# Optimization experiments

Hardware: AMD Instinct MI355X
Metric: run time of the kernel (lower is better)

Reference implementation:

```python
import jax, jax.numpy as jnp
import numpy as np

D_MODEL = 1024
H = 16
D_K = D_MODEL // H
B, S = 4, 2048


def setup_inputs() -> dict:
    key = jax.random.key(0)
    ks = jax.random.split(key, 12)
    std = 1.0 / np.sqrt(D_MODEL)
    inp = {
        "q": jax.random.normal(ks[0], (B, S, D_MODEL), dtype=jnp.float32),
        "k": jax.random.normal(ks[1], (B, S, D_MODEL), dtype=jnp.float32),
        "v": jax.random.normal(ks[2], (B, S, D_MODEL), dtype=jnp.float32),
        "mask": jnp.tril(jnp.ones((S, S), dtype=jnp.int32))[None, None],  # [1,1,S,S] causal
        "w_q": jax.random.normal(ks[3], (D_MODEL, D_MODEL), dtype=jnp.float32) * std,
        "b_q": jax.random.normal(ks[4], (D_MODEL,), dtype=jnp.float32) * std,
        "w_k": jax.random.normal(ks[5], (D_MODEL, D_MODEL), dtype=jnp.float32) * std,
        "b_k": jax.random.normal(ks[6], (D_MODEL,), dtype=jnp.float32) * std,
        "w_v": jax.random.normal(ks[7], (D_MODEL, D_MODEL), dtype=jnp.float32) * std,
        "b_v": jax.random.normal(ks[8], (D_MODEL,), dtype=jnp.float32) * std,
        "w_o": jax.random.normal(ks[9], (D_MODEL, D_MODEL), dtype=jnp.float32) * std,
        "b_o": jax.random.normal(ks[10], (D_MODEL,), dtype=jnp.float32) * std,
    }
    return inp


def reference(q, k, v, mask, w_q, b_q, w_k, b_k, w_v, b_v, w_o, b_o):
    b, s, _ = q.shape
    # linear projections (torch Linear: x @ W^T + b)
    query = q @ w_q.T + b_q
    key_ = k @ w_k.T + b_k
    value = v @ w_v.T + b_v
    # [B,S,D] -> [B,H,S,Dk]
    query = query.reshape(b, s, H, D_K).transpose(0, 2, 1, 3)
    key_ = key_.reshape(b, -1, H, D_K).transpose(0, 2, 1, 3)
    value = value.reshape(b, -1, H, D_K).transpose(0, 2, 1, 3)
    scores = jnp.einsum("bhqd,bhkd->bhqk", query, key_) / jnp.sqrt(jnp.float32(D_K))
    scores = jnp.where(mask == 0, jnp.float32(-1e9), scores)
    attn = jax.nn.softmax(scores, axis=-1)
    out = jnp.einsum("bhqk,bhkd->bhqd", attn, value)
    out = out.transpose(0, 2, 1, 3).reshape(b, s, D_MODEL)
    return out @ w_o.T + b_o
```

## Files before the change

### kernel.cpp

```cpp
#include <hip/hip_runtime.h>


typedef _Float16 h8 __attribute__((ext_vector_type(8)));
typedef float f32x4 __attribute__((ext_vector_type(4)));
typedef float f32x16 __attribute__((ext_vector_type(16)));

#define S_LEN 2048
#define DM 1024
#define DK 64

struct H2 { _Float16 h, l; };
__device__ __forceinline__ H2 split2(float v) {
  H2 r; r.h = (_Float16)v; r.l = (_Float16)(v - (float)r.h); return r;
}
__device__ __forceinline__ unsigned int pack2(float a, float b) {
  union { _Float16 h[2]; unsigned int u; } x;
  x.h[0] = (_Float16)a; x.h[1] = (_Float16)b;
  return x.u;
}

#define GLOAD16(gp, lp)                                                        \
  __builtin_amdgcn_global_load_lds(                                            \
      (const __attribute__((address_space(1))) void*)(gp),                     \
      (__attribute__((address_space(3))) void*)(lp), 16, 0, 0)

__global__ __launch_bounds__(256)
void presplit(const float* __restrict__ X, _Float16* __restrict__ Hi,
              _Float16* __restrict__ Lo, int n8) {
  const int i = blockIdx.x * 256 + threadIdx.x;
  if (i >= n8) return;
  const float4 a = ((const float4*)X)[2 * i];
  const float4 b = ((const float4*)X)[2 * i + 1];
  h8 hv, lv;
  H2 s;
  s = split2(a.x); hv[0] = s.h; lv[0] = s.l;
  s = split2(a.y); hv[1] = s.h; lv[1] = s.l;
  s = split2(a.z); hv[2] = s.h; lv[2] = s.l;
  s = split2(a.w); hv[3] = s.h; lv[3] = s.l;
  s = split2(b.x); hv[4] = s.h; lv[4] = s.l;
  s = split2(b.y); hv[5] = s.h; lv[5] = s.l;
  s = split2(b.z); hv[6] = s.h; lv[6] = s.l;
  s = split2(b.w); hv[7] = s.h; lv[7] = s.l;
  *(h8*)&Hi[(size_t)i * 8] = hv;
  *(h8*)&Lo[(size_t)i * 8] = lv;
}

template<int OUT_MODE>
__global__ __launch_bounds__(256)
void gemm_ps(const _Float16* __restrict__ Xhi, const _Float16* __restrict__ Xlo,
             const _Float16* __restrict__ Whi, const _Float16* __restrict__ Wlo,
             const float* __restrict__ bias,
             _Float16* __restrict__ Yhi, _Float16* __restrict__ Ylo,
             float* __restrict__ Yf) {
  __shared__ _Float16 lds[2][4][128 * 32];
  const int tid = threadIdx.x;
  const int m0 = blockIdx.x * 128, n0 = blockIdx.y * 128;
  const int wid = tid >> 6, lane = tid & 63;
  const int wm = (wid >> 1) * 64, wn = (wid & 1) * 64;
  const int l15 = lane & 15, lg = lane >> 4;
  const _Float16* gsrc = (wid == 0) ? Xhi : (wid == 1) ? Xlo : (wid == 2) ? Whi : Wlo;
  const int rbase = (wid < 2) ? m0 : n0;
  const int rowoff = lane >> 2, coloff = (lane & 3) * 8;
  f32x4 acc[4][4] = {};

  auto stage = [&](int buf, int kt) {
    const int k0 = kt * 32;
#pragma unroll
    for (int c = 0; c < 8; ++c) {
      GLOAD16(&gsrc[(size_t)(rbase + c * 16 + rowoff) * DM + k0 + coloff],
              &lds[buf][wid][c * 512]);
    }
  };

  stage(0, 0);
  __syncthreads();
  for (int kt = 0; kt < 32; ++kt) {
    const int buf = kt & 1;
    if (kt + 1 < 32) stage(buf ^ 1, kt + 1);
    h8 a_h[4], a_l[4], b_h[4], b_l[4];
#pragma unroll
    for (int i = 0; i < 4; ++i) {
      const int ra = (wm + i * 16 + l15) * 32 + lg * 8;
      const int rb = (wn + i * 16 + l15) * 32 + lg * 8;
      a_h[i] = *(const h8*)&lds[buf][0][ra];
      a_l[i] = *(const h8*)&lds[buf][1][ra];
      b_h[i] = *(const h8*)&lds[buf][2][rb];
      b_l[i] = *(const h8*)&lds[buf][3][rb];
    }
    __builtin_amdgcn_s_setprio(1);
#pragma unroll
    for (int mi = 0; mi < 4; ++mi)
#pragma unroll
      for (int ni = 0; ni < 4; ++ni) {
        acc[mi][ni] = __builtin_amdgcn_mfma_f32_16x16x32_f16(a_h[mi], b_h[ni], acc[mi][ni], 0, 0, 0);
        acc[mi][ni] = __builtin_amdgcn_mfma_f32_16x16x32_f16(a_h[mi], b_l[ni], acc[mi][ni], 0, 0, 0);
        acc[mi][ni] = __builtin_amdgcn_mfma_f32_16x16x32_f16(a_l[mi], b_h[ni], acc[mi][ni], 0, 0, 0);
      }
    __builtin_amdgcn_s_setprio(0);
    __syncthreads();
  }
#pragma unroll
  for (int mi = 0; mi < 4; ++mi)
#pragma unroll
    for (int ni = 0; ni < 4; ++ni)
#pragma unroll
      for (int j = 0; j < 4; ++j) {
        const int rg = m0 + wm + mi * 16 + lg * 4 + j;
        const int cg = n0 + wn + ni * 16 + l15;
        const float v = acc[mi][ni][j] + bias[cg];
        if constexpr (OUT_MODE == 0) {
          H2 s = split2(v);
          Yhi[(size_t)rg * DM + cg] = s.h;
          Ylo[(size_t)rg * DM + cg] = s.l;
        } else {
          Yf[(size_t)rg * DM + cg] = v;
        }
      }
}

__global__ __launch_bounds__(256)
void mha_vtrans(const float* __restrict__ Vp,
                _Float16* __restrict__ Vthi, _Float16* __restrict__ Vtlo) {
  __shared__ float tile[64 * 65];
  const int bh = blockIdx.y, s0 = blockIdx.x * 64;
  const int b = bh >> 4, h = bh & 15;
  const int t = threadIdx.x;
  const int row = t >> 2, cg = (t & 3) * 16;
  const size_t inbase = ((size_t)(b * S_LEN + s0 + row)) * DM + h * DK + cg;
#pragma unroll
  for (int i = 0; i < 4; ++i) {
    const float4 v = *(const float4*)&Vp[inbase + i * 4];
    tile[row * 65 + cg + i * 4 + 0] = v.x;
    tile[row * 65 + cg + i * 4 + 1] = v.y;
    tile[row * 65 + cg + i * 4 + 2] = v.z;
    tile[row * 65 + cg + i * 4 + 3] = v.w;
  }
  __syncthreads();
  const int drow = t >> 2, sg = (t & 3) * 16;
  h8 hv0, hv1, lv0, lv1;
#pragma unroll
  for (int i = 0; i < 8; ++i) {
    H2 a = split2(tile[(sg + i) * 65 + drow]);
    hv0[i] = a.h; lv0[i] = a.l;
    H2 c = split2(tile[(sg + 8 + i) * 65 + drow]);
    hv1[i] = c.h; lv1[i] = c.l;
  }
  const size_t ob = ((size_t)bh * DK + drow) * S_LEN + s0 + sg;
  *(h8*)&Vthi[ob] = hv0;
  *(h8*)&Vthi[ob + 8] = hv1;
  *(h8*)&Vtlo[ob] = lv0;
  *(h8*)&Vtlo[ob + 8] = lv1;
}

__global__ __launch_bounds__(64)
void mha_attn(const _Float16* __restrict__ Qhi, const _Float16* __restrict__ Qlo,
              const _Float16* __restrict__ Khi, const _Float16* __restrict__ Klo,
              const _Float16* __restrict__ Vthi, const _Float16* __restrict__ Vtlo,
              _Float16* __restrict__ Ohi, _Float16* __restrict__ Olo) {
  const int lane = threadIdx.x;
  const int l31 = lane & 31, hi = lane >> 5;
  const int hwid = blockIdx.x + (blockIdx.y << 5);
  const int logical = (hwid & 7) * 256 + (hwid >> 3);
  const int r = logical & 31;
  const int bh = logical >> 5;
  const int fq = 63 - r;
  const int b = bh >> 4, h = bh & 15;
  const size_t rowbase = (size_t)b * S_LEN * DM + h * DK;
  const size_t vbase = (size_t)bh * DK * S_LEN;

  h8 qh_r[4], ql_r[4], qh_f[4], ql_f[4];
#pragma unroll
  for (int ks = 0; ks < 4; ++ks) {
    const size_t offr = rowbase + (size_t)(r * 32 + l31) * DM + ks * 16 + hi * 8;
    const size_t offf = rowbase + (size_t)(fq * 32 + l31) * DM + ks * 16 + hi * 8;
    qh_r[ks] = *(const h8*)&Qhi[offr]; ql_r[ks] = *(const h8*)&Qlo[offr];
    qh_f[ks] = *(const h8*)&Qhi[offf]; ql_f[ks] = *(const h8*)&Qlo[offf];
  }
  f32x16 po0r = {}, po1r = {}, po0f = {}, po1f = {};
  float m_r = -1e30f, l_r = 0.0f, m_f = -1e30f, l_f = 0.0f;

  auto loadK = [&](int t, h8 (&kh)[4], h8 (&kl)[4]) {
    const int c0 = t * 32;
#pragma unroll
    for (int ks = 0; ks < 4; ++ks) {
      const size_t koff = rowbase + (size_t)(c0 + l31) * DM + ks * 16 + hi * 8;
      kh[ks] = *(const h8*)&Khi[koff];
      kl[ks] = *(const h8*)&Klo[koff];
    }
  };

  auto smax_pv = [&](const f32x16& sA, const f32x16& sB, bool diag,
                     float& m, float& l, f32x16& po0, f32x16& po1,
                     const h8 (&vh)[2][2], const h8 (&vl)[2][2]) {
    float p[16];
    float tmax = -3e38f;
#pragma unroll
    for (int rr = 0; rr < 16; ++rr) {
      const int kvr = (rr & 3) + 8 * (rr >> 2) + 4 * hi;
      float sv = (sA[rr] + sB[rr]) * 0.125f;
      if (diag && kvr > l31) sv = -1e30f;
      p[rr] = sv;
      tmax = fmaxf(tmax, sv);
    }
    tmax = fmaxf(tmax, __shfl_xor(tmax, 32, 64));
    if (!__all(tmax <= m + 8.0f)) {
      const float mnew = fmaxf(m, tmax);
      const float alpha = __expf(m - mnew);
      l *= alpha;
      po0 = po0 * alpha;
      po1 = po1 * alpha;
      m = mnew;
    }
    float tsum = 0.0f;
#pragma unroll
    for (int rr = 0; rr < 16; ++rr) { p[rr] = __expf(p[rr] - m); tsum += p[rr]; }
    tsum += __shfl_xor(tsum, 32, 64);
    l += tsum;
    unsigned int pw[8], qw[8];
#pragma unroll
    for (int g = 0; g < 8; ++g) pw[g] = pack2(p[2 * g], p[2 * g + 1]);
#pragma unroll
    for (int g = 0; g < 8; ++g) qw[g] = (unsigned int)__shfl_xor((int)pw[g], 32, 64);
    __builtin_amdgcn_s_setprio(1);
#pragma unroll
    for (int cks = 0; cks < 2; ++cks) {
      union { unsigned int u[4]; h8 v; } bp;
      if (hi == 0) {
        bp.u[0] = pw[4 * cks];     bp.u[1] = pw[4 * cks + 1];
        bp.u[2] = qw[4 * cks];     bp.u[3] = qw[4 * cks + 1];
      } else {
        bp.u[0] = qw[4 * cks + 2]; bp.u[1] = qw[4 * cks + 3];
        bp.u[2] = pw[4 * cks + 2]; bp.u[3] = pw[4 * cks + 3];
      }
      po0 = __builtin_amdgcn_mfma_f32_32x32x16_f16(vh[cks][0], bp.v, po0, 0, 0, 0);
      po0 = __builtin_amdgcn_mfma_f32_32x32x16_f16(vl[cks][0], bp.v, po0, 0, 0, 0);
      po1 = __builtin_amdgcn_mfma_f32_32x32x16_f16(vh[cks][1], bp.v, po1, 0, 0, 0);
      po1 = __builtin_amdgcn_mfma_f32_32x32x16_f16(vl[cks][1], bp.v, po1, 0, 0, 0);
    }
    __builtin_amdgcn_s_setprio(0);
  };

  auto body = [&](int t, const h8 (&kh)[4], const h8 (&kl)[4],
                  h8 (&nkh)[4], h8 (&nkl)[4]) {
    const int c0 = t * 32;
    h8 vh[2][2], vl[2][2];
#pragma unroll
    for (int cks = 0; cks < 2; ++cks) {
      const size_t voff = vbase + (size_t)l31 * S_LEN + c0 + cks * 16 + hi * 8;
      vh[cks][0] = *(const h8*)&Vthi[voff];
      vl[cks][0] = *(const h8*)&Vtlo[voff];
      vh[cks][1] = *(const h8*)&Vthi[voff + (size_t)32 * S_LEN];
      vl[cks][1] = *(const h8*)&Vtlo[voff + (size_t)32 * S_LEN];
    }
    if (t + 1 <= fq) loadK(t + 1, nkh, nkl);
    {
      f32x16 sA = {}, sB = {};
      __builtin_amdgcn_s_setprio(1);
#pragma unroll
      for (int ks = 0; ks < 4; ++ks) {
        sA = __builtin_amdgcn_mfma_f32_32x32x16_f16(kh[ks], qh_f[ks], sA, 0, 0, 0);
        sB = __builtin_amdgcn_mfma_f32_32x32x16_f16(kh[ks], ql_f[ks], sB, 0, 0, 0);
        sB = __builtin_amdgcn_mfma_f32_32x32x16_f16(kl[ks], qh_f[ks], sB, 0, 0, 0);
      }
      __builtin_amdgcn_s_setprio(0);
      smax_pv(sA, sB, t == fq, m_f, l_f, po0f, po1f, vh, vl);
    }
    if (t <= r) {
      f32x16 sA = {}, sB = {};
      __builtin_amdgcn_s_setprio(1);
#pragma unroll
      for (int ks = 0; ks < 4; ++ks) {
        sA = __builtin_amdgcn_mfma_f32_32x32x16_f16(kh[ks], qh_r[ks], sA, 0, 0, 0);
        sB = __builtin_amdgcn_mfma_f32_32x32x16_f16(kh[ks], ql_r[ks], sB, 0, 0, 0);
        sB = __builtin_amdgcn_mfma_f32_32x32x16_f16(kl[ks], qh_r[ks], sB, 0, 0, 0);
      }
      __builtin_amdgcn_s_setprio(0);
      smax_pv(sA, sB, t == r, m_r, l_r, po0r, po1r, vh, vl);
    }
  };

  h8 khA[4], klA[4], khB[4], klB[4];
  loadK(0, khA, klA);
  int t = 0;
  while (true) {
    body(t, khA, klA, khB, klB);
    ++t; if (t > fq) break;
    body(t, khB, klB, khA, klA);
    ++t; if (t > fq) break;
  }

  __shared__ float lds_o[32 * 65];
  auto writeO = [&](int qt, float l, const f32x16& po0, const f32x16& po1) {
    const float invl = 1.0f / l;
#pragma unroll
    for (int rr = 0; rr < 16; ++rr) {
      const int dl = (rr & 3) + 8 * (rr >> 2) + 4 * hi;
      lds_o[l31 * 65 + dl] = po0[rr] * invl;
      lds_o[l31 * 65 + 32 + dl] = po1[rr] * invl;
    }
    __syncthreads();
    const size_t ob = ((size_t)b * S_LEN + qt * 32) * DM + h * DK;
    for (int r2 = 0; r2 < 32; ++r2) {
      H2 s = split2(lds_o[r2 * 65 + lane]);
      Ohi[ob + (size_t)r2 * DM + lane] = s.h;
      Olo[ob + (size_t)r2 * DM + lane] = s.l;
    }
    __syncthreads();
  };
  writeO(fq, l_f, po0f, po1f);
  writeO(r, l_r, po0r, po1r);
}

extern "C" void kernel_launch(void* const* d_in, const int* in_sizes, int n_in,
                              void* d_out, int out_size, void* d_ws, size_t ws_size,
                              hipStream_t stream) {
  const float* q   = (const float*)d_in[0];
  const float* k   = (const float*)d_in[1];
  const float* v   = (const float*)d_in[2];
  const float* w_q = (const float*)d_in[4];
  const float* b_q = (const float*)d_in[5];
  const float* w_k = (const float*)d_in[6];
  const float* b_k = (const float*)d_in[7];
  const float* w_v = (const float*)d_in[8];
  const float* b_v = (const float*)d_in[9];
  const float* w_o = (const float*)d_in[10];
  const float* b_o = (const float*)d_in[11];

  const size_t NIN = (size_t)8192 * 1024;
  const size_t NW  = (size_t)1024 * 1024;
  const size_t SZH = NIN * sizeof(_Float16);
  char* ws = (char*)d_ws;
  _Float16* b1 = (_Float16*)(ws + 0 * SZH);
  _Float16* b2 = (_Float16*)(ws + 2 * SZH);
  _Float16* b3 = (_Float16*)(ws + 4 * SZH);
  char*     b4 = ws + 6 * SZH;

  _Float16* Xhi = b1;            _Float16* Xlo = b1 + NIN;
  _Float16* Qph = b2;            _Float16* Qpl = b2 + NIN;
  _Float16* Kph = b3;            _Float16* Kpl = b3 + NIN;
  float*    Vp  = (float*)b4;
  _Float16* Vth = (_Float16*)b1; _Float16* Vtl = (_Float16*)b1 + NIN;
  _Float16* Oh  = (_Float16*)b4; _Float16* Ol  = (_Float16*)b4 + NIN;
  _Float16* Wdh = (_Float16*)d_out; _Float16* Wdl = (_Float16*)d_out + NW;
  _Float16* Woh = (_Float16*)b2;    _Float16* Wol = (_Float16*)b2 + NW;

  const int NIN8 = (int)(NIN / 8), NW8 = (int)(NW / 8);
  dim3 gg(64, 8);

  presplit<<<4096, 256, 0, stream>>>(q, Xhi, Xlo, NIN8);
  presplit<<<512, 256, 0, stream>>>(w_q, Wdh, Wdl, NW8);
  gemm_ps<0><<<gg, 256, 0, stream>>>(Xhi, Xlo, Wdh, Wdl, b_q, Qph, Qpl, nullptr);
  presplit<<<4096, 256, 0, stream>>>(k, Xhi, Xlo, NIN8);
  presplit<<<512, 256, 0, stream>>>(w_k, Wdh, Wdl, NW8);
  gemm_ps<0><<<gg, 256, 0, stream>>>(Xhi, Xlo, Wdh, Wdl, b_k, Kph, Kpl, nullptr);
  presplit<<<4096, 256, 0, stream>>>(v, Xhi, Xlo, NIN8);
  presplit<<<512, 256, 0, stream>>>(w_v, Wdh, Wdl, NW8);
  gemm_ps<1><<<gg, 256, 0, stream>>>(Xhi, Xlo, Wdh, Wdl, b_v, nullptr, nullptr, Vp);
  mha_vtrans<<<dim3(32, 64), 256, 0, stream>>>(Vp, Vth, Vtl);
  mha_attn<<<dim3(32, 64), 64, 0, stream>>>(Qph, Qpl, Kph, Kpl, Vth, Vtl, Oh, Ol);
  presplit<<<512, 256, 0, stream>>>(w_o, Woh, Wol, NW8);
  gemm_ps<1><<<gg, 256, 0, stream>>>(Oh, Ol, Woh, Wol, b_o, nullptr, nullptr, (float*)d_out);
}
```

Measured before the change: 636.4 us.

## Share K/V tiles across four waves via double-buffered swizzled LDS in attention

```diff
diff --git a/kernel.cpp b/kernel.cpp
--- a/kernel.cpp
+++ b/kernel.cpp
@@ -152,22 +152,54 @@
   *(h8*)&Vtlo[ob + 8] = lv1;
 }
 
-__global__ __launch_bounds__(64)
+__global__ __launch_bounds__(256)
 void mha_attn(const _Float16* __restrict__ Qhi, const _Float16* __restrict__ Qlo,
               const _Float16* __restrict__ Khi, const _Float16* __restrict__ Klo,
               const _Float16* __restrict__ Vthi, const _Float16* __restrict__ Vtlo,
               _Float16* __restrict__ Ohi, _Float16* __restrict__ Olo) {
-  const int lane = threadIdx.x;
+  __shared__ int4 smem4[2080];
+  char* smem = (char*)smem4;
+  const int tid = threadIdx.x;
+  const int w = tid >> 6, lane = tid & 63;
   const int l31 = lane & 31, hi = lane >> 5;
-  const int hwid = blockIdx.x + (blockIdx.y << 5);
-  const int logical = (hwid & 7) * 256 + (hwid >> 3);
-  const int r = logical & 31;
-  const int bh = logical >> 5;
+  const int hwid = blockIdx.x + (blockIdx.y << 3);
+  const int logical = (hwid & 7) * 64 + (hwid >> 3);
+  const int bh = logical >> 3, pg = logical & 7;
+  const int r = pg * 4 + w;
   const int fq = 63 - r;
+  const int TMAX = 63 - pg * 4;
   const int b = bh >> 4, h = bh & 15;
   const size_t rowbase = (size_t)b * S_LEN * DM + h * DK;
   const size_t vbase = (size_t)bh * DK * S_LEN;
 
+  const int krow = tid >> 3, kq = tid & 7;
+  const int vd = tid >> 2, vj = tid & 3;
+
+  auto kaddr = [&](int buf, int row, int slot) {
+    return buf * 8192 + row * 256 + ((slot ^ (row & 15)) << 4);
+  };
+  auto vaddr = [&](int buf, int d, int slot) {
+    return 16384 + buf * 8192 + d * 128 + ((slot ^ (d & 7)) << 4);
+  };
+
+  h8 sKh, sKl, sVh, sVl;
+  auto stage_load = [&](int t) {
+    const int c0 = t * 32;
+    const size_t ko = rowbase + (size_t)(c0 + krow) * DM + kq * 8;
+    const size_t vo = vbase + (size_t)vd * S_LEN + c0 + vj * 8;
+    sKh = *(const h8*)&Khi[ko];
+    sKl = *(const h8*)&Klo[ko];
+    sVh = *(const h8*)&Vthi[vo];
+    sVl = *(const h8*)&Vtlo[vo];
+  };
+  auto stage_write = [&](int buf) {
+    *(h8*)(smem + kaddr(buf, krow, kq)) = sKh;
+    *(h8*)(smem + kaddr(buf, krow, kq + 8)) = sKl;
+    *(h8*)(smem + vaddr(buf, vd, vj)) = sVh;
+    *(h8*)(smem + vaddr(buf, vd, vj + 4)) = sVl;
+  };
+
+  stage_load(0);
   h8 qh_r[4], ql_r[4], qh_f[4], ql_f[4];
 #pragma unroll
   for (int ks = 0; ks < 4; ++ks) {
@@ -176,22 +208,14 @@
     qh_r[ks] = *(const h8*)&Qhi[offr]; ql_r[ks] = *(const h8*)&Qlo[offr];
     qh_f[ks] = *(const h8*)&Qhi[offf]; ql_f[ks] = *(const h8*)&Qlo[offf];
   }
+  stage_write(0);
+  __syncthreads();
+
   f32x16 po0r = {}, po1r = {}, po0f = {}, po1f = {};
   float m_r = -1e30f, l_r = 0.0f, m_f = -1e30f, l_f = 0.0f;
 
-  auto loadK = [&](int t, h8 (&kh)[4], h8 (&kl)[4]) {
-    const int c0 = t * 32;
-#pragma unroll
-    for (int ks = 0; ks < 4; ++ks) {
-      const size_t koff = rowbase + (size_t)(c0 + l31) * DM + ks * 16 + hi * 8;
-      kh[ks] = *(const h8*)&Khi[koff];
-      kl[ks] = *(const h8*)&Klo[koff];
-    }
-  };
-
-  auto smax_pv = [&](const f32x16& sA, const f32x16& sB, bool diag,
-                     float& m, float& l, f32x16& po0, f32x16& po1,
-                     const h8 (&vh)[2][2], const h8 (&vl)[2][2]) {
+  auto smax_pv = [&](int buf, const f32x16& sA, const f32x16& sB, bool diag,
+                     float& m, float& l, f32x16& po0, f32x16& po1) {
     float p[16];
     float tmax = -3e38f;
 #pragma unroll
@@ -232,80 +256,79 @@
         bp.u[0] = qw[4 * cks + 2]; bp.u[1] = qw[4 * cks + 3];
         bp.u[2] = pw[4 * cks + 2]; bp.u[3] = pw[4 * cks + 3];
       }
-      po0 = __builtin_amdgcn_mfma_f32_32x32x16_f16(vh[cks][0], bp.v, po0, 0, 0, 0);
-      po0 = __builtin_amdgcn_mfma_f32_32x32x16_f16(vl[cks][0], bp.v, po0, 0, 0, 0);
-      po1 = __builtin_amdgcn_mfma_f32_32x32x16_f16(vh[cks][1], bp.v, po1, 0, 0, 0);
-      po1 = __builtin_amdgcn_mfma_f32_32x32x16_f16(vl[cks][1], bp.v, po1, 0, 0, 0);
+      const h8 vh0 = *(const h8*)(smem + vaddr(buf, l31, 2 * cks + hi));
+      const h8 vl0 = *(const h8*)(smem + vaddr(buf, l31, 4 + 2 * cks + hi));
+      const h8 vh1 = *(const h8*)(smem + vaddr(buf, l31 + 32, 2 * cks + hi));
+      const h8 vl1 = *(const h8*)(smem + vaddr(buf, l31 + 32, 4 + 2 * cks + hi));
+      po0 = __builtin_amdgcn_mfma_f32_32x32x16_f16(vh0, bp.v, po0, 0, 0, 0);
+      po0 = __builtin_amdgcn_mfma_f32_32x32x16_f16(vl0, bp.v, po0, 0, 0, 0);
+      po1 = __builtin_amdgcn_mfma_f32_32x32x16_f16(vh1, bp.v, po1, 0, 0, 0);
+      po1 = __builtin_amdgcn_mfma_f32_32x32x16_f16(vl1, bp.v, po1, 0, 0, 0);
     }
     __builtin_amdgcn_s_setprio(0);
   };
 
-  auto body = [&](int t, const h8 (&kh)[4], const h8 (&kl)[4],
-                  h8 (&nkh)[4], h8 (&nkl)[4]) {
-    const int c0 = t * 32;
-    h8 vh[2][2], vl[2][2];
-#pragma unroll
-    for (int cks = 0; cks < 2; ++cks) {
-      const size_t voff = vbase + (size_t)l31 * S_LEN + c0 + cks * 16 + hi * 8;
-      vh[cks][0] = *(const h8*)&Vthi[voff];
-      vl[cks][0] = *(const h8*)&Vtlo[voff];
-      vh[cks][1] = *(const h8*)&Vthi[voff + (size_t)32 * S_LEN];
-      vl[cks][1] = *(const h8*)&Vtlo[voff + (size_t)32 * S_LEN];
-    }
-    if (t + 1 <= fq) loadK(t + 1, nkh, nkl);
-    {
-      f32x16 sA = {}, sB = {};
-      __builtin_amdgcn_s_setprio(1);
+  for (int t = 0; t <= TMAX; ++t) {
+    const int buf = t & 1;
+    if (t < TMAX) stage_load(t + 1);
+    if (t <= fq) {
+      h8 kh[4], kl[4];
 #pragma unroll
       for (int ks = 0; ks < 4; ++ks) {
-        sA = __builtin_amdgcn_mfma_f32_32x32x16_f16(kh[ks], qh_f[ks], sA, 0, 0, 0);
-        sB = __builtin_amdgcn_mfma_f32_32x32x16_f16(kh[ks], ql_f[ks], sB, 0, 0, 0);
-        sB = __builtin_amdgcn_mfma_f32_32x32x16_f16(kl[ks], qh_f[ks], sB, 0, 0, 0);
-      }
-      __builtin_amdgcn_s_setprio(0);
-      smax_pv(sA, sB, t == fq, m_f, l_f, po0f, po1f, vh, vl);
-    }
-    if (t <= r) {
-      f32x16 sA = {}, sB = {};
-      __builtin_amdgcn_s_setprio(1);
-#pragma unroll
-      for (int ks = 0; ks < 4; ++ks) {
-        sA = __builtin_amdgcn_mfma_f32_32x32x16_f16(kh[ks], qh_r[ks], sA, 0, 0, 0);
-        sB = __builtin_amdgcn_mfma_f32_32x32x16_f16(kh[ks], ql_r[ks], sB, 0, 0, 0);
-        sB = __builtin_amdgcn_mfma_f32_32x32x16_f16(kl[ks], qh_r[ks], sB, 0, 0, 0);
-      }
-      __builtin_amdgcn_s_setprio(0);
-      smax_pv(sA, sB, t == r, m_r, l_r, po0r, po1r, vh, vl);
-    }
-  };
-
-  h8 khA[4], klA[4], khB[4], klB[4];
-  loadK(0, khA, klA);
-  int t = 0;
-  while (true) {
-    body(t, khA, klA, khB, klB);
-    ++t; if (t > fq) break;
-    body(t, khB, klB, khA, klA);
-    ++t; if (t > fq) break;
-  }
-
-  __shared__ float lds_o[32 * 65];
+        kh[ks] = *(const h8*)(smem + kaddr(buf, l31, 2 * ks + hi));
+        kl[ks] = *(const h8*)(smem + kaddr(buf, l31, 8 + 2 * ks + hi));
+      }
+      {
+        f32x16 sA = {}, sB = {};
+        __builtin_amdgcn_s_setprio(1);
+#pragma unroll
+        for (int ks = 0; ks < 4; ++ks) {
+          sA = __builtin_amdgcn_mfma_f32_32x32x16_f16(kh[ks], qh_f[ks], sA, 0, 0, 0);
+          sB = __builtin_amdgcn_mfma_f32_32x32x16_f16(kh[ks], ql_f[ks], sB, 0, 0, 0);
+          sB = __builtin_amdgcn_mfma_f32_32x32x16_f16(kl[ks], qh_f[ks], sB, 0, 0, 0);
+        }
+        __builtin_amdgcn_s_setprio(0);
+        smax_pv(buf, sA, sB, t == fq, m_f, l_f, po0f, po1f);
+      }
+      if (t <= r) {
+        f32x16 sA = {}, sB = {};
+        __builtin_amdgcn_s_setprio(1);
+#pragma unroll
+        for (int ks = 0; ks < 4; ++ks) {
+          sA = __builtin_amdgcn_mfma_f32_32x32x16_f16(kh[ks], qh_r[ks], sA, 0, 0, 0);
+          sB = __builtin_amdgcn_mfma_f32_32x32x16_f16(kh[ks], ql_r[ks], sB, 0, 0, 0);
+          sB = __builtin_amdgcn_mfma_f32_32x32x16_f16(kl[ks], qh_r[ks], sB, 0, 0, 0);
+        }
+        __builtin_amdgcn_s_setprio(0);
+        smax_pv(buf, sA, sB, t == r, m_r, l_r, po0r, po1r);
+      }
+    }
+    __syncthreads();
+    if (t < TMAX) stage_write(buf ^ 1);
+    __syncthreads();
+  }
+
+  unsigned int* outl = (unsigned int*)(smem + w * 8320);
   auto writeO = [&](int qt, float l, const f32x16& po0, const f32x16& po1) {
     const float invl = 1.0f / l;
 #pragma unroll
     for (int rr = 0; rr < 16; ++rr) {
       const int dl = (rr & 3) + 8 * (rr >> 2) + 4 * hi;
-      lds_o[l31 * 65 + dl] = po0[rr] * invl;
-      lds_o[l31 * 65 + 32 + dl] = po1[rr] * invl;
-    }
-    __syncthreads();
+      H2 s0 = split2(po0[rr] * invl);
+      H2 s1 = split2(po1[rr] * invl);
+      union { _Float16 f[2]; unsigned int u; } x0, x1;
+      x0.f[0] = s0.h; x0.f[1] = s0.l;
+      x1.f[0] = s1.h; x1.f[1] = s1.l;
+      outl[l31 * 65 + dl] = x0.u;
+      outl[l31 * 65 + 32 + dl] = x1.u;
+    }
     const size_t ob = ((size_t)b * S_LEN + qt * 32) * DM + h * DK;
     for (int r2 = 0; r2 < 32; ++r2) {
-      H2 s = split2(lds_o[r2 * 65 + lane]);
-      Ohi[ob + (size_t)r2 * DM + lane] = s.h;
-      Olo[ob + (size_t)r2 * DM + lane] = s.l;
-    }
-    __syncthreads();
+      union { unsigned int u; _Float16 f[2]; } x;
+      x.u = outl[r2 * 65 + lane];
+      Ohi[ob + (size_t)r2 * DM + lane] = x.f[0];
+      Olo[ob + (size_t)r2 * DM + lane] = x.f[1];
+    }
   };
   writeO(fq, l_f, po0f, po1f);
   writeO(r, l_r, po0r, po1r);
@@ -357,7 +380,7 @@
   presplit<<<512, 256, 0, stream>>>(w_v, Wdh, Wdl, NW8);
   gemm_ps<1><<<gg, 256, 0, stream>>>(Xhi, Xlo, Wdh, Wdl, b_v, nullptr, nullptr, Vp);
   mha_vtrans<<<dim3(32, 64), 256, 0, stream>>>(Vp, Vth, Vtl);
-  mha_attn<<<dim3(32, 64), 64, 0, stream>>>(Qph, Qpl, Kph, Kpl, Vth, Vtl, Oh, Ol);
+  mha_attn<<<dim3(8, 64), 256, 0, stream>>>(Qph, Qpl, Kph, Kpl, Vth, Vtl, Oh, Ol);
   presplit<<<512, 256, 0, stream>>>(w_o, Woh, Wol, NW8);
   gemm_ps<1><<<gg, 256, 0, stream>>>(Oh, Ol, Woh, Wol, b_o, nullptr, nullptr, (float*)d_out);
 }
```

Result: no change. 643.3 us (+1.1%).
